# Kernel optimization log

Measured on AMD Instinct MI355X. Metric: run time of the kernel, lower is better.

The kernel has to match this reference:

```python
import jax, jax.numpy as jnp
import numpy as np

NODE_DIM = 128
NUM_IRREPS = 224          # 128 + 64 + 32 gates (one per irrep channel)
SPH_DIM = 480             # 128*1 + 64*3 + 32*5
HIDDEN = NODE_DIM + 2 * NUM_IRREPS  # 576
NUM_BASIS = 20
N_NODES = 10000
N_EDGES = 160000
# Each gate scalar is broadcast over its irrep's (2l+1) components.
_REPEATS = np.array([1] * 128 + [3] * 64 + [5] * 32)


def _expand_gate(g):
    # [E, 224] -> [E, 480], repeating each gate over its irrep dimension
    return jnp.repeat(g, _REPEATS, axis=-1, total_repeat_length=SPH_DIM)


def setup_inputs() -> dict:
    key = jax.random.key(0)
    ks = jax.random.split(key, 12)
    x_scalar = jax.random.normal(ks[0], (N_NODES, NODE_DIM), dtype=jnp.float32)
    x_spherical = jax.random.normal(ks[1], (N_NODES, SPH_DIM), dtype=jnp.float32)
    rbf = jax.random.uniform(ks[2], (N_EDGES, NUM_BASIS), dtype=jnp.float32)
    fcut = jax.random.uniform(ks[3], (N_EDGES, 1), dtype=jnp.float32)
    rsh = jax.random.normal(ks[4], (N_EDGES, SPH_DIM), dtype=jnp.float32)
    edge_index = jax.random.randint(ks[5], (2, N_EDGES), 0, N_NODES, dtype=jnp.int64)
    s1 = 1.0 / np.sqrt(NODE_DIM)
    s2 = 1.0 / np.sqrt(NUM_BASIS)
    W1 = jax.random.uniform(ks[6], (NODE_DIM, NODE_DIM), jnp.float32, -s1, s1)
    b1 = jnp.zeros((NODE_DIM,), jnp.float32)
    W2 = jax.random.uniform(ks[7], (NODE_DIM, HIDDEN), jnp.float32, -s1, s1)
    b2 = jnp.zeros((HIDDEN,), jnp.float32)
    Wr = jax.random.uniform(ks[8], (NUM_BASIS, HIDDEN), jnp.float32, -s2, s2)
    br = jnp.zeros((HIDDEN,), jnp.float32)
    return {"x_scalar": x_scalar, "x_spherical": x_spherical, "rbf": rbf,
            "fcut": fcut, "rsh": rsh, "edge_index": edge_index,
            "W1": W1, "b1": b1, "W2": W2, "b2": b2, "Wr": Wr, "br": br}


def reference(x_scalar, x_spherical, rbf, fcut, rsh, edge_index,
              W1, b1, W2, b2, Wr, br):
    src, dst = edge_index[0], edge_index[1]
    # scalar MLP: Linear -> SiLU -> Linear
    scalar_out = jax.nn.silu(x_scalar @ W1 + b1) @ W2 + b2          # [N, 576]
    filter_weight = (rbf @ Wr + br) * fcut                          # [E, 576]
    filter_out = scalar_out[dst] * filter_weight                    # [E, 576]
    gate_state = filter_out[:, :NUM_IRREPS]                         # [E, 224]
    gate_edge = filter_out[:, NUM_IRREPS:2 * NUM_IRREPS]            # [E, 224]
    message_scalar = filter_out[:, 2 * NUM_IRREPS:]                 # [E, 128]
    # ElementwiseTensorProduct(edge_irreps, '224x0e'): per-channel scalar gating
    message_spherical = (x_spherical[dst] * _expand_gate(gate_state)
                         + rsh * _expand_gate(gate_edge))           # [E, 480]
    new_scalar = x_scalar.at[src].add(message_scalar)
    new_spherical = x_spherical.at[src].add(message_spherical)
    return (new_scalar, new_spherical)
```

## Files before the change

kernel.cpp:

```cpp
#include <hip/hip_runtime.h>

#define NODE_DIM 128
#define NUM_IRREPS 224
#define SPH_DIM 480
#define HIDDEN 576
#define NUM_BASIS 20
#define N_NODES 10000
#define N_EDGES 160000
#define NPB 4

__global__ void init_out(const float* __restrict__ xs,
                         const float* __restrict__ xsp,
                         float* __restrict__ out,
                         int* __restrict__ counts) {
    const int stride = gridDim.x * blockDim.x;
    const int t0 = blockIdx.x * blockDim.x + threadIdx.x;
    for (int i = t0; i < N_NODES * NODE_DIM; i += stride) out[i] = xs[i];
    float* o2 = out + (size_t)N_NODES * NODE_DIM;
    for (int i = t0; i < N_NODES * SPH_DIM; i += stride) o2[i] = xsp[i];
    for (int i = t0; i < N_NODES; i += stride) counts[i] = 0;
}

__global__ __launch_bounds__(128) void node_mlp(
    const float* __restrict__ x,
    const float* __restrict__ W1, const float* __restrict__ b1,
    const float* __restrict__ W2, const float* __restrict__ b2,
    float* __restrict__ so) {
    __shared__ float xs[NPB][NODE_DIM];
    __shared__ float hs[NPB][NODE_DIM];
    const int tid = threadIdx.x;
    const int n0 = blockIdx.x * NPB;

    #pragma unroll
    for (int n = 0; n < NPB; ++n) {
        int node = n0 + n;
        xs[n][tid] = (node < N_NODES) ? x[(size_t)node * NODE_DIM + tid] : 0.f;
    }
    __syncthreads();

    float acc[NPB];
    #pragma unroll
    for (int n = 0; n < NPB; ++n) acc[n] = b1[tid];
    for (int k = 0; k < NODE_DIM; ++k) {
        float w = W1[k * NODE_DIM + tid];
        #pragma unroll
        for (int n = 0; n < NPB; ++n) acc[n] = fmaf(xs[n][k], w, acc[n]);
    }
    #pragma unroll
    for (int n = 0; n < NPB; ++n) {
        float v = acc[n];
        hs[n][tid] = v / (1.f + __expf(-v));
    }
    __syncthreads();

    for (int j = tid; j < HIDDEN; j += 128) {
        float a2[NPB];
        #pragma unroll
        for (int n = 0; n < NPB; ++n) a2[n] = b2[j];
        for (int k = 0; k < NODE_DIM; ++k) {
            float w = W2[k * HIDDEN + j];
            #pragma unroll
            for (int n = 0; n < NPB; ++n) a2[n] = fmaf(hs[n][k], w, a2[n]);
        }
        #pragma unroll
        for (int n = 0; n < NPB; ++n) {
            int node = n0 + n;
            if (node < N_NODES) so[(size_t)node * HIDDEN + j] = a2[n];
        }
    }
}

__global__ __launch_bounds__(256) void hist_kernel(const int* __restrict__ eidx,
                                                   int* __restrict__ counts) {
    int i = blockIdx.x * blockDim.x + threadIdx.x;
    if (i < N_EDGES) atomicAdd(&counts[eidx[i]], 1);
}

__global__ __launch_bounds__(1024) void scan_kernel(const int* __restrict__ counts,
                                                    int* __restrict__ offsets,
                                                    int* __restrict__ cursor) {
    __shared__ int s[1024];
    const int tid = threadIdx.x;
    int vals[10];
    int run = 0;
    #pragma unroll
    for (int i = 0; i < 10; ++i) {
        int idx = tid * 10 + i;
        int c = (idx < N_NODES) ? counts[idx] : 0;
        vals[i] = run;
        run += c;
    }
    s[tid] = run;
    __syncthreads();
    for (int off = 1; off < 1024; off <<= 1) {
        int t = (tid >= off) ? s[tid - off] : 0;
        __syncthreads();
        if (tid >= off) s[tid] += t;
        __syncthreads();
    }
    int base = (tid > 0) ? s[tid - 1] : 0;
    #pragma unroll
    for (int i = 0; i < 10; ++i) {
        int idx = tid * 10 + i;
        if (idx < N_NODES) {
            int v = base + vals[i];
            offsets[idx] = v;
            cursor[idx] = v;
        }
    }
    if (tid == 1023) offsets[N_NODES] = s[1023];
}

__global__ __launch_bounds__(256) void scatter_kernel(const int* __restrict__ eidx,
                                                      int* __restrict__ cursor,
                                                      int* __restrict__ edge_order) {
    int i = blockIdx.x * blockDim.x + threadIdx.x;
    if (i < N_EDGES) {
        int s = eidx[i];
        int pos = atomicAdd(&cursor[s], 1);
        edge_order[pos] = i;
    }
}

__global__ __launch_bounds__(256) void node_gather(
    const float* __restrict__ xsp,
    const float* __restrict__ rbf, const float* __restrict__ fcut,
    const float* __restrict__ rsh, const int* __restrict__ eidx,
    const float* __restrict__ Wr, const float* __restrict__ br,
    const float* __restrict__ so,
    const int* __restrict__ offsets, const int* __restrict__ edge_order,
    float* __restrict__ out_scalar, float* __restrict__ out_sph)
{
    const int t = threadIdx.x;
    const int n = blockIdx.x;
    const bool dup  = (t >= 224);
    const int  r    = dup ? (t - 32) : t;
    const int  j0   = r;
    const int  j1   = NUM_IRREPS + r;
    const bool has2 = (t < 128);
    const int  j2   = 2 * NUM_IRREPS + t;

    int nd, d0;
    if (t < 128)      { nd = 1; d0 = t; }
    else if (t < 192) { nd = 3; d0 = 128 + (t - 128) * 3; }
    else if (t < 224) { nd = 3; d0 = 320 + (t - 192) * 5; }
    else              { nd = 2; d0 = 320 + (t - 224) * 5 + 3; }

    float wr0[NUM_BASIS], wr1[NUM_BASIS], wr2[NUM_BASIS];
    #pragma unroll
    for (int k = 0; k < NUM_BASIS; ++k) {
        wr0[k] = Wr[k * HIDDEN + j0];
        wr1[k] = Wr[k * HIDDEN + j1];
        wr2[k] = has2 ? Wr[k * HIDDEN + j2] : 0.f;
    }
    const float br0 = br[j0], br1 = br[j1], br2 = has2 ? br[j2] : 0.f;

    const int beg = offsets[n];
    const int end = offsets[n + 1];

    float accS = 0.f, accD0 = 0.f, accD1 = 0.f, accD2 = 0.f;

    if (beg < end) {
        int   e   = edge_order[beg];
        int   dst = eidx[N_EDGES + e];
        float fc  = fcut[e];
        const float4* r4 = (const float4*)(rbf + (size_t)e * NUM_BASIS);
        float4 q0 = r4[0], q1 = r4[1], q2 = r4[2], q3 = r4[3], q4 = r4[4];

        for (int idx = beg; idx < end; ++idx) {
            const int   ce   = e;
            const int   cdst = dst;
            const float cfc  = fc;
            const float rb[NUM_BASIS] = {q0.x,q0.y,q0.z,q0.w, q1.x,q1.y,q1.z,q1.w,
                                         q2.x,q2.y,q2.z,q2.w, q3.x,q3.y,q3.z,q3.w,
                                         q4.x,q4.y,q4.z,q4.w};
            if (idx + 1 < end) {
                e   = edge_order[idx + 1];
                dst = eidx[N_EDGES + e];
                fc  = fcut[e];
                r4  = (const float4*)(rbf + (size_t)e * NUM_BASIS);
                q0 = r4[0]; q1 = r4[1]; q2 = r4[2]; q3 = r4[3]; q4 = r4[4];
            }

            float a0 = br0, a1 = br1;
            #pragma unroll
            for (int k = 0; k < NUM_BASIS; ++k) {
                a0 = fmaf(rb[k], wr0[k], a0);
                a1 = fmaf(rb[k], wr1[k], a1);
            }
            const float* sod = so + (size_t)cdst * HIDDEN;
            const float fo0 = a0 * cfc * sod[j0];
            const float fo1 = a1 * cfc * sod[j1];
            if (has2) {
                float a2 = br2;
                #pragma unroll
                for (int k = 0; k < NUM_BASIS; ++k) a2 = fmaf(rb[k], wr2[k], a2);
                accS = fmaf(a2 * cfc, sod[j2], accS);
            }
            const float* xd = xsp + (size_t)cdst * SPH_DIM + d0;
            const float* rd = rsh + (size_t)ce  * SPH_DIM + d0;
            accD0 = fmaf(xd[0], fo0, fmaf(rd[0], fo1, accD0));
            if (nd > 1) accD1 = fmaf(xd[1], fo0, fmaf(rd[1], fo1, accD1));
            if (nd > 2) accD2 = fmaf(xd[2], fo0, fmaf(rd[2], fo1, accD2));
        }
    }

    if (t < 128) out_scalar[(size_t)n * NODE_DIM + t] += accS;
    float* od = out_sph + (size_t)n * SPH_DIM + d0;
    od[0] += accD0;
    if (nd > 1) od[1] += accD1;
    if (nd > 2) od[2] += accD2;
}

extern "C" void kernel_launch(void* const* d_in, const int* in_sizes, int n_in,
                              void* d_out, int out_size, void* d_ws, size_t ws_size,
                              hipStream_t stream) {
    const float* x_scalar    = (const float*)d_in[0];
    const float* x_spherical = (const float*)d_in[1];
    const float* rbf         = (const float*)d_in[2];
    const float* fcut        = (const float*)d_in[3];
    const float* rsh         = (const float*)d_in[4];
    const int*   eidx        = (const int*)d_in[5];
    const float* W1          = (const float*)d_in[6];
    const float* b1          = (const float*)d_in[7];
    const float* W2          = (const float*)d_in[8];
    const float* b2          = (const float*)d_in[9];
    const float* Wr          = (const float*)d_in[10];
    const float* br          = (const float*)d_in[11];

    float* out        = (float*)d_out;
    float* out_scalar = out;
    float* out_sph    = out + (size_t)N_NODES * NODE_DIM;

    float* scalar_out = (float*)d_ws;
    int*   counts     = (int*)(scalar_out + (size_t)N_NODES * HIDDEN);
    int*   offsets    = counts + N_NODES;
    int*   cursor     = offsets + N_NODES + 1;
    int*   edge_order = cursor + N_NODES;

    init_out<<<2048, 256, 0, stream>>>(x_scalar, x_spherical, out, counts);
    hist_kernel<<<(N_EDGES + 255) / 256, 256, 0, stream>>>(eidx, counts);
    scan_kernel<<<1, 1024, 0, stream>>>(counts, offsets, cursor);
    scatter_kernel<<<(N_EDGES + 255) / 256, 256, 0, stream>>>(eidx, cursor, edge_order);
    node_mlp<<<(N_NODES + NPB - 1) / NPB, 128, 0, stream>>>(x_scalar, W1, b1, W2, b2, scalar_out);
    node_gather<<<N_NODES, 256, 0, stream>>>(x_spherical, rbf, fcut, rsh, eidx,
                                             Wr, br, scalar_out, offsets, edge_order,
                                             out_scalar, out_sph);
}
```

Baseline: 334.9 us.

## Deepen edge prefetch pipeline in node_gather, use wave-shuffle scan, widen MLP node tile

The gather loop now prefetches edge indices several edges ahead and loads the whole next edge's payload (rbf, scalar-out, xsp, rsh values) before the current one is used, so dependent global-load latency overlaps with compute. The scan kernel replaces the shared-memory Hillis-Steele loop with wavefront shuffle scans plus a small cross-wave step, cutting barriers. The node MLP processes 8 nodes per block instead of 4, and node_gather gets an occupancy hint. The deeper prefetch costs more registers and issues redundant clamped loads near the end of each edge list.

New measurement: 335.5 us. No clear change (+0.2%).

```diff
diff --git a/kernel.cpp b/kernel.cpp
--- a/kernel.cpp
+++ b/kernel.cpp
@@ -7,7 +7,7 @@
 #define NUM_BASIS 20
 #define N_NODES 10000
 #define N_EDGES 160000
-#define NPB 4
+#define NPB 8
 
 __global__ void init_out(const float* __restrict__ xs,
                          const float* __restrict__ xsp,
@@ -79,7 +79,7 @@
 __global__ __launch_bounds__(1024) void scan_kernel(const int* __restrict__ counts,
                                                     int* __restrict__ offsets,
                                                     int* __restrict__ cursor) {
-    __shared__ int s[1024];
+    __shared__ int wsum[16];
     const int tid = threadIdx.x;
     int vals[10];
     int run = 0;
@@ -90,15 +90,27 @@
         vals[i] = run;
         run += c;
     }
-    s[tid] = run;
-    __syncthreads();
-    for (int off = 1; off < 1024; off <<= 1) {
-        int t = (tid >= off) ? s[tid - off] : 0;
-        __syncthreads();
-        if (tid >= off) s[tid] += t;
-        __syncthreads();
-    }
-    int base = (tid > 0) ? s[tid - 1] : 0;
+    const int lane = tid & 63, w = tid >> 6;
+    int inc = run;
+    #pragma unroll
+    for (int off = 1; off < 64; off <<= 1) {
+        int v = __shfl_up(inc, off);
+        if (lane >= off) inc += v;
+    }
+    if (lane == 63) wsum[w] = inc;
+    __syncthreads();
+    if (w == 0) {
+        int v = (lane < 16) ? wsum[lane] : 0;
+        #pragma unroll
+        for (int off = 1; off < 16; off <<= 1) {
+            int u = __shfl_up(v, off);
+            if (lane >= off) v += u;
+        }
+        if (lane < 16) wsum[lane] = v;
+    }
+    __syncthreads();
+    const int wbase = (w > 0) ? wsum[w - 1] : 0;
+    const int base = wbase + inc - run;
     #pragma unroll
     for (int i = 0; i < 10; ++i) {
         int idx = tid * 10 + i;
@@ -108,7 +120,7 @@
             cursor[idx] = v;
         }
     }
-    if (tid == 1023) offsets[N_NODES] = s[1023];
+    if (tid == 1023) offsets[N_NODES] = wbase + inc;
 }
 
 __global__ __launch_bounds__(256) void scatter_kernel(const int* __restrict__ eidx,
@@ -122,7 +134,28 @@
     }
 }
 
-__global__ __launch_bounds__(256) void node_gather(
+#define DOT20(a, WREG) do { \
+    a = fmaf(q0.x, WREG[0], a);  a = fmaf(q0.y, WREG[1], a);  a = fmaf(q0.z, WREG[2], a);  a = fmaf(q0.w, WREG[3], a); \
+    a = fmaf(q1.x, WREG[4], a);  a = fmaf(q1.y, WREG[5], a);  a = fmaf(q1.z, WREG[6], a);  a = fmaf(q1.w, WREG[7], a); \
+    a = fmaf(q2.x, WREG[8], a);  a = fmaf(q2.y, WREG[9], a);  a = fmaf(q2.z, WREG[10], a); a = fmaf(q2.w, WREG[11], a); \
+    a = fmaf(q3.x, WREG[12], a); a = fmaf(q3.y, WREG[13], a); a = fmaf(q3.z, WREG[14], a); a = fmaf(q3.w, WREG[15], a); \
+    a = fmaf(q4.x, WREG[16], a); a = fmaf(q4.y, WREG[17], a); a = fmaf(q4.z, WREG[18], a); a = fmaf(q4.w, WREG[19], a); \
+} while (0)
+
+#define LOAD_PAYLOAD() do { \
+    const float4* rq = (const float4*)(rbf + (size_t)eC * NUM_BASIS); \
+    q0 = rq[0]; q1 = rq[1]; q2 = rq[2]; q3 = rq[3]; q4 = rq[4]; \
+    const float* sod = so + (size_t)dC * HIDDEN; \
+    s0 = sod[j0]; s1 = sod[j1]; \
+    if (has2) s2 = sod[j2]; \
+    const float* xd = xsp + (size_t)dC * SPH_DIM + d0; \
+    const float* rd = rsh + (size_t)eC * SPH_DIM + d0; \
+    x0 = xd[0]; r0 = rd[0]; \
+    if (nd > 1) { x1 = xd[1]; r1 = rd[1]; } \
+    if (nd > 2) { x2 = xd[2]; r2 = rd[2]; } \
+} while (0)
+
+__global__ __launch_bounds__(256, 4) void node_gather(
     const float* __restrict__ xsp,
     const float* __restrict__ rbf, const float* __restrict__ fcut,
     const float* __restrict__ rsh, const int* __restrict__ eidx,
@@ -138,7 +171,7 @@
     const int  j0   = r;
     const int  j1   = NUM_IRREPS + r;
     const bool has2 = (t < 128);
-    const int  j2   = 2 * NUM_IRREPS + t;
+    const int  j2   = 2 * NUM_IRREPS + (t & 127);
 
     int nd, d0;
     if (t < 128)      { nd = 1; d0 = t; }
@@ -155,53 +188,46 @@
     }
     const float br0 = br[j0], br1 = br[j1], br2 = has2 ? br[j2] : 0.f;
 
-    const int beg = offsets[n];
-    const int end = offsets[n + 1];
+    const int beg  = offsets[n];
+    const int end_ = offsets[n + 1];
 
     float accS = 0.f, accD0 = 0.f, accD1 = 0.f, accD2 = 0.f;
 
-    if (beg < end) {
-        int   e   = edge_order[beg];
-        int   dst = eidx[N_EDGES + e];
-        float fc  = fcut[e];
-        const float4* r4 = (const float4*)(rbf + (size_t)e * NUM_BASIS);
-        float4 q0 = r4[0], q1 = r4[1], q2 = r4[2], q3 = r4[3], q4 = r4[4];
-
-        for (int idx = beg; idx < end; ++idx) {
-            const int   ce   = e;
-            const int   cdst = dst;
-            const float cfc  = fc;
-            const float rb[NUM_BASIS] = {q0.x,q0.y,q0.z,q0.w, q1.x,q1.y,q1.z,q1.w,
-                                         q2.x,q2.y,q2.z,q2.w, q3.x,q3.y,q3.z,q3.w,
-                                         q4.x,q4.y,q4.z,q4.w};
-            if (idx + 1 < end) {
-                e   = edge_order[idx + 1];
-                dst = eidx[N_EDGES + e];
-                fc  = fcut[e];
-                r4  = (const float4*)(rbf + (size_t)e * NUM_BASIS);
-                q0 = r4[0]; q1 = r4[1]; q2 = r4[2]; q3 = r4[3]; q4 = r4[4];
-            }
-
-            float a0 = br0, a1 = br1;
-            #pragma unroll
-            for (int k = 0; k < NUM_BASIS; ++k) {
-                a0 = fmaf(rb[k], wr0[k], a0);
-                a1 = fmaf(rb[k], wr1[k], a1);
-            }
-            const float* sod = so + (size_t)cdst * HIDDEN;
-            const float fo0 = a0 * cfc * sod[j0];
-            const float fo1 = a1 * cfc * sod[j1];
-            if (has2) {
-                float a2 = br2;
-                #pragma unroll
-                for (int k = 0; k < NUM_BASIS; ++k) a2 = fmaf(rb[k], wr2[k], a2);
-                accS = fmaf(a2 * cfc, sod[j2], accS);
-            }
-            const float* xd = xsp + (size_t)cdst * SPH_DIM + d0;
-            const float* rd = rsh + (size_t)ce  * SPH_DIM + d0;
-            accD0 = fmaf(xd[0], fo0, fmaf(rd[0], fo1, accD0));
-            if (nd > 1) accD1 = fmaf(xd[1], fo0, fmaf(rd[1], fo1, accD1));
-            if (nd > 2) accD2 = fmaf(xd[2], fo0, fmaf(rd[2], fo1, accD2));
+    if (beg < end_) {
+        const int last = end_ - 1;
+        const int i1 = min(beg + 1, last);
+        const int i2 = min(beg + 2, last);
+        const int i3 = min(beg + 3, last);
+        int   eC = edge_order[beg];
+        int   e1 = edge_order[i1];
+        int   e2 = edge_order[i2];
+        int   e3 = edge_order[i3];
+        int   dC = eidx[N_EDGES + eC]; float fC = fcut[eC];
+        int   d1 = eidx[N_EDGES + e1]; float f1 = fcut[e1];
+        int   d2 = eidx[N_EDGES + e2]; float f2 = fcut[e2];
+
+        float4 q0, q1, q2, q3, q4;
+        float  s0, s1, s2 = 0.f, x0, x1 = 0.f, x2 = 0.f, r0, r1 = 0.f, r2 = 0.f;
+        LOAD_PAYLOAD();
+
+        for (int idx = beg; idx <= last; ++idx) {
+            float a0 = br0, a1 = br1, a2 = br2;
+            DOT20(a0, wr0);
+            DOT20(a1, wr1);
+            if (has2) { DOT20(a2, wr2); }
+            const float fo0 = a0 * fC * s0;
+            const float fo1 = a1 * fC * s1;
+            if (has2) accS = fmaf(a2 * fC, s2, accS);
+            accD0 = fmaf(x0, fo0, fmaf(r0, fo1, accD0));
+            if (nd > 1) accD1 = fmaf(x1, fo0, fmaf(r1, fo1, accD1));
+            if (nd > 2) accD2 = fmaf(x2, fo0, fmaf(r2, fo1, accD2));
+
+            eC = e1; dC = d1; fC = f1;
+            e1 = e2; d1 = d2; f1 = f2;
+            LOAD_PAYLOAD();
+            e2 = e3;
+            d2 = eidx[N_EDGES + e3]; f2 = fcut[e3];
+            e3 = edge_order[min(idx + 4, last)];
         }
     }
 
```

## Process sorted edges in fixed windows with shared filter staging and run-length atomics

Applied to the files above, without the earlier changes.

Replaces the one-block-per-node gather with blocks that each handle a fixed window of 64 source-sorted edges. Filter outputs for 16-edge chunks are staged in shared memory, and channels are remapped so each thread reads contiguous sph columns. Per-node partial sums are flushed with atomics whenever the source changes. The scan now uses wavefront shuffles, and node_mlp handles 8 nodes per block. This is meant to fix load imbalance from variable node degree and improve coalescing, at the cost of atomics at window boundaries and extra syncs.

Result: slower. 483.3 us (+44.3%).

```diff
diff --git a/kernel.cpp b/kernel.cpp
--- a/kernel.cpp
+++ b/kernel.cpp
@@ -7,7 +7,9 @@
 #define NUM_BASIS 20
 #define N_NODES 10000
 #define N_EDGES 160000
-#define NPB 4
+#define NPB 8
+#define EB 64
+#define CH 16
 
 __global__ void init_out(const float* __restrict__ xs,
                          const float* __restrict__ xsp,
@@ -79,7 +81,7 @@
 __global__ __launch_bounds__(1024) void scan_kernel(const int* __restrict__ counts,
                                                     int* __restrict__ offsets,
                                                     int* __restrict__ cursor) {
-    __shared__ int s[1024];
+    __shared__ int wsum[16];
     const int tid = threadIdx.x;
     int vals[10];
     int run = 0;
@@ -90,15 +92,27 @@
         vals[i] = run;
         run += c;
     }
-    s[tid] = run;
-    __syncthreads();
-    for (int off = 1; off < 1024; off <<= 1) {
-        int t = (tid >= off) ? s[tid - off] : 0;
-        __syncthreads();
-        if (tid >= off) s[tid] += t;
-        __syncthreads();
-    }
-    int base = (tid > 0) ? s[tid - 1] : 0;
+    const int lane = tid & 63, w = tid >> 6;
+    int inc = run;
+    #pragma unroll
+    for (int off = 1; off < 64; off <<= 1) {
+        int v = __shfl_up(inc, off);
+        if (lane >= off) inc += v;
+    }
+    if (lane == 63) wsum[w] = inc;
+    __syncthreads();
+    if (w == 0) {
+        int v = (lane < 16) ? wsum[lane] : 0;
+        #pragma unroll
+        for (int off = 1; off < 16; off <<= 1) {
+            int u = __shfl_up(v, off);
+            if (lane >= off) v += u;
+        }
+        if (lane < 16) wsum[lane] = v;
+    }
+    __syncthreads();
+    const int wbase = (w > 0) ? wsum[w - 1] : 0;
+    const int base = wbase + inc - run;
     #pragma unroll
     for (int i = 0; i < 10; ++i) {
         int idx = tid * 10 + i;
@@ -108,108 +122,124 @@
             cursor[idx] = v;
         }
     }
-    if (tid == 1023) offsets[N_NODES] = s[1023];
+    if (tid == 1023) offsets[N_NODES] = wbase + inc;
 }
 
 __global__ __launch_bounds__(256) void scatter_kernel(const int* __restrict__ eidx,
                                                       int* __restrict__ cursor,
-                                                      int* __restrict__ edge_order) {
+                                                      int* __restrict__ edge_order,
+                                                      int* __restrict__ edge_src) {
     int i = blockIdx.x * blockDim.x + threadIdx.x;
     if (i < N_EDGES) {
         int s = eidx[i];
         int pos = atomicAdd(&cursor[s], 1);
         edge_order[pos] = i;
-    }
-}
-
-__global__ __launch_bounds__(256) void node_gather(
+        edge_src[pos] = s;
+    }
+}
+
+__global__ __launch_bounds__(256, 1) void edge_win(
     const float* __restrict__ xsp,
     const float* __restrict__ rbf, const float* __restrict__ fcut,
     const float* __restrict__ rsh, const int* __restrict__ eidx,
     const float* __restrict__ Wr, const float* __restrict__ br,
     const float* __restrict__ so,
-    const int* __restrict__ offsets, const int* __restrict__ edge_order,
+    const int* __restrict__ edge_order, const int* __restrict__ edge_src,
     float* __restrict__ out_scalar, float* __restrict__ out_sph)
 {
+    __shared__ float rbf_s[EB][NUM_BASIS];
+    __shared__ float fo_s[CH][HIDDEN + 8];
+    __shared__ int   e_s[EB];
+    __shared__ int   src_s[EB];
+    __shared__ int   dst_s[EB];
+    __shared__ float fc_s[EB];
+
     const int t = threadIdx.x;
-    const int n = blockIdx.x;
-    const bool dup  = (t >= 224);
-    const int  r    = dup ? (t - 32) : t;
-    const int  j0   = r;
-    const int  j1   = NUM_IRREPS + r;
-    const bool has2 = (t < 128);
-    const int  j2   = 2 * NUM_IRREPS + t;
-
-    int nd, d0;
-    if (t < 128)      { nd = 1; d0 = t; }
-    else if (t < 192) { nd = 3; d0 = 128 + (t - 128) * 3; }
-    else if (t < 224) { nd = 3; d0 = 320 + (t - 192) * 5; }
-    else              { nd = 2; d0 = 320 + (t - 224) * 5 + 3; }
-
-    float wr0[NUM_BASIS], wr1[NUM_BASIS], wr2[NUM_BASIS];
+    const int base = blockIdx.x * EB;
+
+    const bool has3 = (t < 64);
+    const int c_a = t, c_b = 256 + t, c_c = 512 + t;
+
+    float wA[NUM_BASIS], wB[NUM_BASIS], wC[NUM_BASIS];
     #pragma unroll
     for (int k = 0; k < NUM_BASIS; ++k) {
-        wr0[k] = Wr[k * HIDDEN + j0];
-        wr1[k] = Wr[k * HIDDEN + j1];
-        wr2[k] = has2 ? Wr[k * HIDDEN + j2] : 0.f;
-    }
-    const float br0 = br[j0], br1 = br[j1], br2 = has2 ? br[j2] : 0.f;
-
-    const int beg = offsets[n];
-    const int end = offsets[n + 1];
-
-    float accS = 0.f, accD0 = 0.f, accD1 = 0.f, accD2 = 0.f;
-
-    if (beg < end) {
-        int   e   = edge_order[beg];
-        int   dst = eidx[N_EDGES + e];
-        float fc  = fcut[e];
-        const float4* r4 = (const float4*)(rbf + (size_t)e * NUM_BASIS);
-        float4 q0 = r4[0], q1 = r4[1], q2 = r4[2], q3 = r4[3], q4 = r4[4];
-
-        for (int idx = beg; idx < end; ++idx) {
-            const int   ce   = e;
-            const int   cdst = dst;
-            const float cfc  = fc;
+        wA[k] = Wr[k * HIDDEN + c_a];
+        wB[k] = Wr[k * HIDDEN + c_b];
+        wC[k] = has3 ? Wr[k * HIDDEN + c_c] : 0.f;
+    }
+    const float bA = br[c_a], bB = br[c_b], bC = has3 ? br[c_c] : 0.f;
+
+    if (t < EB) {
+        int pos = base + t;
+        int e = edge_order[pos];
+        e_s[t]   = e;
+        src_s[t] = edge_src[pos];
+        dst_s[t] = eidx[N_EDGES + e];
+        fc_s[t]  = fcut[e];
+    }
+    __syncthreads();
+    for (int i = t; i < EB * NUM_BASIS; i += 256) {
+        int le = i / NUM_BASIS, k = i - le * NUM_BASIS;
+        rbf_s[le][k] = rbf[(size_t)e_s[le] * NUM_BASIS + k];
+    }
+
+    const int g1i = (t < 128) ? t : (128 + (t - 128) / 3);
+    const int g2i = (t < 64) ? (128 + (128 + t) / 3) : (192 + (t - 64) / 5);
+
+    float accS = 0.f, accD1 = 0.f, accD2 = 0.f;
+    __syncthreads();
+    int cur_src = src_s[0];
+
+    for (int c = 0; c < EB / CH; ++c) {
+        for (int le = 0; le < CH; ++le) {
+            const int e = c * CH + le;
+            const int dst = dst_s[e];
+            const float fc = fc_s[e];
+            const float* sod = so + (size_t)dst * HIDDEN;
+            const float4* rq = (const float4*)rbf_s[e];
+            float4 q0 = rq[0], q1 = rq[1], q2 = rq[2], q3 = rq[3], q4 = rq[4];
+            float a0 = bA, a1 = bB, a2 = bC;
             const float rb[NUM_BASIS] = {q0.x,q0.y,q0.z,q0.w, q1.x,q1.y,q1.z,q1.w,
                                          q2.x,q2.y,q2.z,q2.w, q3.x,q3.y,q3.z,q3.w,
                                          q4.x,q4.y,q4.z,q4.w};
-            if (idx + 1 < end) {
-                e   = edge_order[idx + 1];
-                dst = eidx[N_EDGES + e];
-                fc  = fcut[e];
-                r4  = (const float4*)(rbf + (size_t)e * NUM_BASIS);
-                q0 = r4[0]; q1 = r4[1]; q2 = r4[2]; q3 = r4[3]; q4 = r4[4];
-            }
-
-            float a0 = br0, a1 = br1;
             #pragma unroll
             for (int k = 0; k < NUM_BASIS; ++k) {
-                a0 = fmaf(rb[k], wr0[k], a0);
-                a1 = fmaf(rb[k], wr1[k], a1);
+                a0 = fmaf(rb[k], wA[k], a0);
+                a1 = fmaf(rb[k], wB[k], a1);
+                a2 = fmaf(rb[k], wC[k], a2);
             }
-            const float* sod = so + (size_t)cdst * HIDDEN;
-            const float fo0 = a0 * cfc * sod[j0];
-            const float fo1 = a1 * cfc * sod[j1];
-            if (has2) {
-                float a2 = br2;
-                #pragma unroll
-                for (int k = 0; k < NUM_BASIS; ++k) a2 = fmaf(rb[k], wr2[k], a2);
-                accS = fmaf(a2 * cfc, sod[j2], accS);
+            fo_s[le][c_a] = a0 * fc * sod[c_a];
+            fo_s[le][c_b] = a1 * fc * sod[c_b];
+            if (has3) fo_s[le][c_c] = a2 * fc * sod[c_c];
+        }
+        __syncthreads();
+        for (int le = 0; le < CH; ++le) {
+            const int e = c * CH + le;
+            const int s = src_s[e];
+            if (s != cur_src) {
+                atomicAdd(&out_sph[(size_t)cur_src * SPH_DIM + t], accD1);
+                if (t < 224) atomicAdd(&out_sph[(size_t)cur_src * SPH_DIM + 256 + t], accD2);
+                if (t < 128) atomicAdd(&out_scalar[(size_t)cur_src * NODE_DIM + t], accS);
+                accD1 = accD2 = accS = 0.f;
+                cur_src = s;
             }
-            const float* xd = xsp + (size_t)cdst * SPH_DIM + d0;
-            const float* rd = rsh + (size_t)ce  * SPH_DIM + d0;
-            accD0 = fmaf(xd[0], fo0, fmaf(rd[0], fo1, accD0));
-            if (nd > 1) accD1 = fmaf(xd[1], fo0, fmaf(rd[1], fo1, accD1));
-            if (nd > 2) accD2 = fmaf(xd[2], fo0, fmaf(rd[2], fo1, accD2));
-        }
-    }
-
-    if (t < 128) out_scalar[(size_t)n * NODE_DIM + t] += accS;
-    float* od = out_sph + (size_t)n * SPH_DIM + d0;
-    od[0] += accD0;
-    if (nd > 1) od[1] += accD1;
-    if (nd > 2) od[2] += accD2;
+            const int dst = dst_s[e];
+            const int eg  = e_s[e];
+            const float xv1 = xsp[(size_t)dst * SPH_DIM + t];
+            const float rv1 = rsh[(size_t)eg  * SPH_DIM + t];
+            accD1 = fmaf(xv1, fo_s[le][g1i], fmaf(rv1, fo_s[le][NUM_IRREPS + g1i], accD1));
+            if (t < 224) {
+                const float xv2 = xsp[(size_t)dst * SPH_DIM + 256 + t];
+                const float rv2 = rsh[(size_t)eg  * SPH_DIM + 256 + t];
+                accD2 = fmaf(xv2, fo_s[le][g2i], fmaf(rv2, fo_s[le][NUM_IRREPS + g2i], accD2));
+            }
+            if (t < 128) accS += fo_s[le][2 * NUM_IRREPS + t];
+        }
+        __syncthreads();
+    }
+    atomicAdd(&out_sph[(size_t)cur_src * SPH_DIM + t], accD1);
+    if (t < 224) atomicAdd(&out_sph[(size_t)cur_src * SPH_DIM + 256 + t], accD2);
+    if (t < 128) atomicAdd(&out_scalar[(size_t)cur_src * NODE_DIM + t], accS);
 }
 
 extern "C" void kernel_launch(void* const* d_in, const int* in_sizes, int n_in,
@@ -237,13 +267,14 @@
     int*   offsets    = counts + N_NODES;
     int*   cursor     = offsets + N_NODES + 1;
     int*   edge_order = cursor + N_NODES;
+    int*   edge_src   = edge_order + N_EDGES;
 
     init_out<<<2048, 256, 0, stream>>>(x_scalar, x_spherical, out, counts);
     hist_kernel<<<(N_EDGES + 255) / 256, 256, 0, stream>>>(eidx, counts);
     scan_kernel<<<1, 1024, 0, stream>>>(counts, offsets, cursor);
-    scatter_kernel<<<(N_EDGES + 255) / 256, 256, 0, stream>>>(eidx, cursor, edge_order);
+    scatter_kernel<<<(N_EDGES + 255) / 256, 256, 0, stream>>>(eidx, cursor, edge_order, edge_src);
     node_mlp<<<(N_NODES + NPB - 1) / NPB, 128, 0, stream>>>(x_scalar, W1, b1, W2, b2, scalar_out);
-    node_gather<<<N_NODES, 256, 0, stream>>>(x_spherical, rbf, fcut, rsh, eidx,
-                                             Wr, br, scalar_out, offsets, edge_order,
-                                             out_scalar, out_sph);
-}
+    edge_win<<<N_EDGES / EB, 256, 0, stream>>>(x_spherical, rbf, fcut, rsh, eidx,
+                                               Wr, br, scalar_out, edge_order, edge_src,
+                                               out_scalar, out_sph);
+}
```
